# Performance work log

Hardware: AMD Instinct MI355X
Metric: run time of the kernel (lower is better)

## Reference

```python
import jax, jax.numpy as jnp
import numpy as np

B, S, NB, ORDER, D = 256, 50, 8, 2, 128
N_ITEMS, N_RELS = 100000, 200
STDV = 1.0 / float(np.sqrt(D))  # reset_parameters: uniform(-1/sqrt(hidden), 1/sqrt(hidden))


def setup_inputs() -> dict:
    key = jax.random.key(0)
    ks = jax.random.split(key, 24)
    u = lambda k, shape: jax.random.uniform(k, shape, jnp.float32, -STDV, STDV)
    return {
        'h_iids': jax.random.randint(ks[0], (B, S), 1, N_ITEMS),
        'a_iids': jax.random.randint(ks[1], (B,), 0, N_ITEMS),
        'adj_entity': jax.random.randint(ks[2], (N_ITEMS, NB), 0, N_ITEMS),
        'adj_relation': jax.random.randint(ks[3], (N_ITEMS, NB), 0, N_RELS),
        'item_emb': u(ks[4], (N_ITEMS, D)),
        'rel_emb': u(ks[5], (N_RELS, D)),
        'Wa': u(ks[6], (D, 1)), 'ba': u(ks[7], (1,)),          # linear_attention
        'Wt': u(ks[8], (D, D)), 'bt': u(ks[9], (D,)),          # linear_attention_transform
        'Wih': u(ks[10], (D, 3 * D)), 'Whh': u(ks[11], (D, 3 * D)),  # GRU (1 layer)
        'bih': u(ks[12], (3 * D,)), 'bhh': u(ks[13], (3 * D,)),
        'W1': u(ks[14], (D, D)), 'b1': u(ks[15], (D,)),        # linear_one
        'W2': u(ks[16], (D, D)), 'b2': u(ks[17], (D,)),        # linear_two
        'W3': u(ks[18], (D, 1)),                               # linear_three (no bias)
        'Wtr': u(ks[19], (2 * D, D)), 'btr': u(ks[20], (D,)),  # linear_transform
    }


def _forward(h_iids, adj_entity, adj_relation, item_emb, rel_emb,
             Wa, ba, Wt, bt, Wih, Whh, bih, bhh,
             W1, b1, W2, b2, W3, Wtr, btr):
    # ---- get_neighbors: multi-hop KG neighbor expansion ----
    entities = [h_iids]           # level 0: [B, S]
    relations = []
    for i in range(ORDER):
        e = entities[i]
        entities.append(adj_entity[e].reshape(B, -1))    # [B, S*NB^(i+1)]
        relations.append(adj_relation[e].reshape(B, -1))
    ent_embs = [item_emb[e] for e in entities]           # gathers
    rel_embs = [rel_emb[r] for r in relations]
    # ---- high_order_aggregate: attention-weighted neighbor aggregation ----
    neib = ent_embs[ORDER]                                # [B, S*NB^ORDER, D]
    for i in range(ORDER):
        self_e = ent_embs[ORDER - i - 1]                  # [B, M, D]
        rel = rel_embs[ORDER - i - 1].reshape(B, -1, NB, D)
        nb4 = neib.reshape(rel.shape)                     # [B, M, NB, D]
        att = (self_e[:, :, None, :] * rel * nb4) @ Wa + ba   # [B, M, NB, 1]
        alpha = jax.nn.softmax(att, axis=2)
        agg = jnp.sum(nb4 * alpha, axis=2)                # [B, M, D]
        neib = (self_e + agg) @ Wt + bt                   # aggregate='sum' branch
    item_embs = neib                                      # [B, S, D] (sigmoid in src is dead code)
    # ---- GRU, 1 layer, batch_first ----
    def step(h, x):
        gi = x @ Wih + bih
        gh = h @ Whh + bhh
        ir, iz, inn = jnp.split(gi, 3, axis=-1)
        hr, hz, hn = jnp.split(gh, 3, axis=-1)
        r = jax.nn.sigmoid(ir + hr)
        z = jax.nn.sigmoid(iz + hz)
        n = jnp.tanh(inn + r * hn)
        h2 = (1.0 - z) * n + z * h
        return h2, h2
    h0 = jnp.zeros((B, D), jnp.float32)
    _, outs = jax.lax.scan(step, h0, jnp.swapaxes(item_embs, 0, 1))
    output = jnp.swapaxes(outs, 0, 1)                     # [B, S, D]
    # ---- attention pooling over sequence ----
    last_idx = jnp.clip(jnp.sum(h_iids != 0, axis=1) - 1, 0, S - 1)
    local_ht = output[jnp.arange(B), last_idx]            # [B, D]
    q1 = (local_ht @ W1 + b1)[:, None, :]
    q2 = output @ W2 + b2
    al = jax.nn.sigmoid(q1 + q2) @ W3                     # [B, S, 1]
    global_ht = jnp.sum(al * output, axis=1)
    ght = jnp.concatenate([local_ht, global_ht], axis=1) @ Wtr + btr
    logits = jax.nn.relu(ght @ item_emb.T)                # [B, n_items]
    return logits


def reference(h_iids, a_iids, adj_entity, adj_relation, item_emb, rel_emb,
              Wa, ba, Wt, bt, Wih, Whh, bih, bhh,
              W1, b1, W2, b2, W3, Wtr, btr):
    # a_iids is accepted by forward() but unused (matches the torch source).
    return _forward(h_iids, adj_entity, adj_relation, item_emb, rel_emb,
                    Wa, ba, Wt, bt, Wih, Whh, bih, bhh,
                    W1, b1, W2, b2, W3, Wtr, btr)
```

## Files before the change

### kernel.cpp

```cpp
#include <hip/hip_runtime.h>
#include <hip/hip_bf16.h>
#include <math.h>

#define NB_B 256
#define NB_S 50
#define NB_NB 8
#define NB_D 128
#define NB_NITEMS 100000

#define C_RZ (-1.442695041f)
#define C_N (2.885390082f)

typedef __attribute__((ext_vector_type(8))) short short8;
typedef __attribute__((ext_vector_type(4))) float f32x4;
typedef unsigned int uint;
typedef unsigned short ushort;

__device__ __forceinline__ ushort f2bf(float f) {
  union { float f; uint u; } v;
  v.f = f;
  return (ushort)((v.u + 0x7fffu + ((v.u >> 16) & 1u)) >> 16);
}
__device__ __forceinline__ uint packbf(float a, float b) {
  return (uint)f2bf(a) | ((uint)f2bf(b) << 16);
}
__device__ __forceinline__ float bflo(uint u) {
  union { uint u; float f; } v; v.u = u << 16; return v.f;
}
__device__ __forceinline__ float bfhi(uint u) {
  union { uint u; float f; } v; v.u = u & 0xffff0000u; return v.f;
}
__device__ __forceinline__ float bf2f(ushort u) {
  union { uint u; float f; } v; v.u = (uint)u << 16; return v.f;
}
__device__ __forceinline__ void unpack8(uint4 u, float* f) {
  f[0] = bflo(u.x); f[1] = bfhi(u.x);
  f[2] = bflo(u.y); f[3] = bfhi(u.y);
  f[4] = bflo(u.z); f[5] = bfhi(u.z);
  f[6] = bflo(u.w); f[7] = bfhi(u.w);
}

__device__ __forceinline__ void castf_body(const float* __restrict__ src,
                                           uint* __restrict__ dst, int i, int n8) {
  if (i >= n8) return;
  float4 a = ((const float4*)src)[2 * i];
  float4 b = ((const float4*)src)[2 * i + 1];
  uint4 o;
  o.x = packbf(a.x, a.y);
  o.y = packbf(a.z, a.w);
  o.z = packbf(b.x, b.y);
  o.w = packbf(b.z, b.w);
  ((uint4*)dst)[i] = o;
}
template <int CO, bool SCALED>
__device__ __forceinline__ void castT_body(const float* __restrict__ W,
                                           ushort* __restrict__ WT, int idx) {
  if (idx >= 128 * CO) return;
  int n = idx >> 7, k = idx & 127;
  float v = W[(size_t)k * CO + n];
  if (SCALED) v *= (n < 256 ? C_RZ : C_N);
  WT[idx] = f2bf(v);
}
__global__ __launch_bounds__(256) void prep_kernel(
    const float* __restrict__ item_emb, const float* __restrict__ rel_emb,
    const float* __restrict__ Wt, const float* __restrict__ Wih,
    const float* __restrict__ Whh, const float* __restrict__ W2,
    const float* __restrict__ bih, const float* __restrict__ bhh,
    const int* __restrict__ h_iids, const int* __restrict__ adj_e,
    const int* __restrict__ adj_r, uint* __restrict__ EMB_BF,
    uint* __restrict__ REL_BF, ushort* __restrict__ WtT,
    ushort* __restrict__ WihT, ushort* __restrict__ WhhT,
    ushort* __restrict__ W2T, float* __restrict__ GIBIAS,
    int* __restrict__ E0, int* __restrict__ E2, int* __restrict__ RK,
    int* __restrict__ RK1) {
  int bx = blockIdx.x, tid = threadIdx.x;
  if (bx < 6250) {
    castf_body(item_emb, EMB_BF, bx * 256 + tid, 1600000);
  } else if (bx < 6263) {
    castf_body(rel_emb, REL_BF, (bx - 6250) * 256 + tid, 3200);
  } else if (bx < 6327) {
    castT_body<128, false>(Wt, WtT, (bx - 6263) * 256 + tid);
  } else if (bx < 6519) {
    castT_body<384, true>(Wih, WihT, (bx - 6327) * 256 + tid);
  } else if (bx < 6711) {
    castT_body<384, true>(Whh, WhhT, (bx - 6519) * 256 + tid);
  } else if (bx < 6775) {
    castT_body<128, false>(W2, W2T, (bx - 6711) * 256 + tid);
  } else if (bx < 6776) {
    if (tid < 256) GIBIAS[tid] = C_RZ * (bih[tid] + bhh[tid]);
  } else if (bx < 6777) {
    int idx = 256 + tid;
    if (idx < 384) GIBIAS[idx] = C_N * bih[idx];
  } else if (bx < 7177) {
    int p = (bx - 6777) * 256 + tid;
    if (p < NB_B * NB_S * NB_NB) {
      int b = p / (NB_S * NB_NB);
      int m = p % (NB_S * NB_NB);
      int h = h_iids[b * NB_S + (m >> 3)];
      int e = adj_e[h * NB_NB + (m & 7)];
      E0[p] = e;
      int4 ea = ((const int4*)(adj_e + (size_t)e * 8))[0];
      int4 eb = ((const int4*)(adj_e + (size_t)e * 8))[1];
      int4 ra = ((const int4*)(adj_r + (size_t)e * 8))[0];
      int4 rb = ((const int4*)(adj_r + (size_t)e * 8))[1];
      ((int4*)(E2 + (size_t)p * 8))[0] = ea;
      ((int4*)(E2 + (size_t)p * 8))[1] = eb;
      ((int4*)(RK + (size_t)p * 8))[0] = ra;
      ((int4*)(RK + (size_t)p * 8))[1] = rb;
    }
  } else {
    int p = (bx - 7177) * 256 + tid;
    if (p < NB_B * NB_S) {
      int e = h_iids[p];
      int4 ra = ((const int4*)(adj_r + (size_t)e * 8))[0];
      int4 rb = ((const int4*)(adj_r + (size_t)e * 8))[1];
      ((int4*)(RK1 + (size_t)p * 8))[0] = ra;
      ((int4*)(RK1 + (size_t)p * 8))[1] = rb;
    }
  }
}

__device__ __forceinline__ uint4 hop_pair4(
    int e_self, int q, int p, const int* __restrict__ E2d,
    const int* __restrict__ RKd, const uint* __restrict__ embB,
    const uint* __restrict__ relB, const uint* __restrict__ neibB,
    const float* __restrict__ Wa, float* __restrict__ alds) {
  uint4 us = ((const uint4*)(embB + (size_t)e_self * 64))[q];
  float s[8], wa[8], sw[8];
  unpack8(us, s);
  *(float4*)&wa[0] = ((const float4*)Wa)[q * 2];
  *(float4*)&wa[4] = ((const float4*)Wa)[q * 2 + 1];
#pragma unroll
  for (int d = 0; d < 8; d++) sw[d] = s[d] * wa[d];

  int4 ra = ((const int4*)(RKd + (size_t)p * 8))[0];
  int4 rb = ((const int4*)(RKd + (size_t)p * 8))[1];
  int rk[8] = {ra.x, ra.y, ra.z, ra.w, rb.x, rb.y, rb.z, rb.w};

  uint4 nbp[8];
  if (neibB == nullptr) {
    int4 ea = ((const int4*)(E2d + (size_t)p * 8))[0];
    int4 eb = ((const int4*)(E2d + (size_t)p * 8))[1];
    int e2[8] = {ea.x, ea.y, ea.z, ea.w, eb.x, eb.y, eb.z, eb.w};
#pragma unroll
    for (int k = 0; k < 8; k++)
      nbp[k] = ((const uint4*)(embB + (size_t)e2[k] * 64))[q];
  } else {
#pragma unroll
    for (int k = 0; k < 8; k++)
      nbp[k] = ((const uint4*)(neibB + ((size_t)p * 8 + k) * 64))[q];
  }

  float t[8];
#pragma unroll
  for (int k = 0; k < 8; k++) {
    uint4 ur = ((const uint4*)(relB + (size_t)rk[k] * 64))[q];
    float rr[8], nb[8];
    unpack8(ur, rr);
    unpack8(nbp[k], nb);
    float tt = 0.f;
#pragma unroll
    for (int d = 0; d < 8; d++) tt = fmaf(sw[d] * rr[d], nb[d], tt);
    t[k] = tt;
  }

  bool b0 = (q & 1), b1 = (q & 2), b2 = (q & 4);
  float a4[4];
#pragma unroll
  for (int i = 0; i < 4; i++) {
    float send = b0 ? t[i] : t[4 + i];
    float recv = __shfl_xor(send, 1);
    a4[i] = (b0 ? t[4 + i] : t[i]) + recv;
  }
  float a2[2];
#pragma unroll
  for (int i = 0; i < 2; i++) {
    float send = b1 ? a4[i] : a4[2 + i];
    float recv = __shfl_xor(send, 2);
    a2[i] = (b1 ? a4[2 + i] : a4[i]) + recv;
  }
  float send1 = b2 ? a2[0] : a2[1];
  float recv1 = __shfl_xor(send1, 4);
  float c = (b2 ? a2[1] : a2[0]) + recv1;
  c += __shfl_xor(c, 8);

  float e = __expf(c);
  float den = e;
  den += __shfl_xor(den, 1);
  den += __shfl_xor(den, 2);
  den += __shfl_xor(den, 4);
  float alpha = e * __builtin_amdgcn_rcpf(den);

  int kstar = (q & 1) * 4 + (q & 2) + ((q & 4) >> 2);
  if (q < 8) alds[kstar] = alpha;
  asm volatile("s_waitcnt lgkmcnt(0)" ::: "memory");
  float a8[8];
  *(float4*)&a8[0] = ((const float4*)alds)[0];
  *(float4*)&a8[4] = ((const float4*)alds)[1];

  float x[8];
#pragma unroll
  for (int d = 0; d < 8; d++) x[d] = s[d];
#pragma unroll
  for (int k = 0; k < 8; k++) {
    float nb[8];
    unpack8(nbp[k], nb);
#pragma unroll
    for (int d = 0; d < 8; d++) x[d] = fmaf(a8[k], nb[d], x[d]);
  }
  uint4 o;
  o.x = packbf(x[0], x[1]);
  o.y = packbf(x[2], x[3]);
  o.z = packbf(x[4], x[5]);
  o.w = packbf(x[6], x[7]);
  return o;
}

__global__ __launch_bounds__(256) void hoplin_kernel(
    const int* __restrict__ E0, const int* __restrict__ E2,
    const int* __restrict__ RK, const uint* __restrict__ embB,
    const uint* __restrict__ relB, const float* __restrict__ Wa,
    const ushort* __restrict__ WtT, const float* __restrict__ bt,
    ushort* __restrict__ NEIB) {
  __shared__ ushort X0s[16 * 128];
  __shared__ float als[16][8];
  const int bx = blockIdx.x;
  const int wv = threadIdx.x >> 6, ln = threadIdx.x & 63;
  const int g = ln >> 4, q = ln & 15;
  const int lp = wv * 4 + g;
  const int p = bx * 16 + lp;

  int e_self = E0[p];
  uint4 o = hop_pair4(e_self, q, p, E2, RK, embB, relB, nullptr, Wa, als[lp]);
  {
    int byte = (lp * 256 + q * 16) ^ ((lp & 7) << 4);
    *(uint4*)((char*)X0s + byte) = o;
  }
  __syncthreads();

  const int lr = ln & 15, lg = ln >> 4;
  short8 afr[4];
#pragma unroll
  for (int kf = 0; kf < 4; kf++) {
    int byte = (lr * 256 + lg * 16 + kf * 64) ^ ((lr & 7) << 4);
    afr[kf] = *(const short8*)((const char*)X0s + byte);
  }
  f32x4 acc[2] = {};
#pragma unroll
  for (int nf = 0; nf < 2; nf++) {
    int n = (wv * 2 + nf) * 16 + lr;
    const ushort* bb = WtT + (size_t)n * 128 + lg * 8;
#pragma unroll
    for (int kf = 0; kf < 4; kf++) {
      short8 bv = *(const short8*)(bb + kf * 32);
      acc[nf] = __builtin_amdgcn_mfma_f32_16x16x32_bf16(afr[kf], bv, acc[nf],
                                                        0, 0, 0);
    }
  }
#pragma unroll
  for (int nf = 0; nf < 2; nf++) {
    int n = (wv * 2 + nf) * 16 + lr;
    float bv = bt[n];
#pragma unroll
    for (int r = 0; r < 4; r++) {
      int mg = bx * 16 + lg * 4 + r;
      NEIB[(size_t)mg * 128 + n] = f2bf(acc[nf][r] + bv);
    }
  }
}

__global__ __launch_bounds__(256) void hopgi_kernel(
    const int* __restrict__ h_iids, const int* __restrict__ RK1,
    const uint* __restrict__ embB, const uint* __restrict__ relB,
    const uint* __restrict__ neibB, const float* __restrict__ Wa,
    const ushort* __restrict__ WtT, const float* __restrict__ bt,
    const ushort* __restrict__ WihT, const float* __restrict__ GIBIAS,
    float* __restrict__ GI) {
  __shared__ ushort X1s[16 * 128];
  __shared__ ushort SEQs[16 * 128];
  __shared__ float als[16][8];
  const int wv = threadIdx.x >> 6, ln = threadIdx.x & 63;
  const int g = ln >> 4, q = ln & 15;
  const int lp = wv * 4 + g;
  const int p = blockIdx.x * 16 + lp;

  int e_self = h_iids[p];
  uint4 o = hop_pair4(e_self, q, p, nullptr, RK1, embB, relB, neibB, Wa, als[lp]);
  {
    int byte = (lp * 256 + q * 16) ^ ((lp & 7) << 4);
    *(uint4*)((char*)X1s + byte) = o;
  }
  __syncthreads();

  const int lr = ln & 15, lg = ln >> 4;
  {
    short8 afr[4];
#pragma unroll
    for (int kf = 0; kf < 4; kf++) {
      int byte = (lr * 256 + lg * 16 + kf * 64) ^ ((lr & 7) << 4);
      afr[kf] = *(const short8*)((const char*)X1s + byte);
    }
    f32x4 acc[2] = {};
#pragma unroll
    for (int nf = 0; nf < 2; nf++) {
      int n = (wv * 2 + nf) * 16 + lr;
      const ushort* bb = WtT + (size_t)n * 128 + lg * 8;
#pragma unroll
      for (int kf = 0; kf < 4; kf++) {
        short8 b = *(const short8*)(bb + kf * 32);
        acc[nf] = __builtin_amdgcn_mfma_f32_16x16x32_bf16(afr[kf], b, acc[nf],
                                                          0, 0, 0);
      }
    }
#pragma unroll
    for (int nf = 0; nf < 2; nf++) {
      int n = (wv * 2 + nf) * 16 + lr;
      float bv = bt[n];
#pragma unroll
      for (int r = 0; r < 4; r++) {
        int m = lg * 4 + r;
        int byte = (m * 256 + n * 2) ^ ((m & 7) << 4);
        *(ushort*)((char*)SEQs + byte) = f2bf(acc[nf][r] + bv);
      }
    }
  }
  __syncthreads();

  {
    short8 sfr[4];
#pragma unroll
    for (int kf = 0; kf < 4; kf++) {
      int byte = (lr * 256 + lg * 16 + kf * 64) ^ ((lr & 7) << 4);
      sfr[kf] = *(const short8*)((const char*)SEQs + byte);
    }
#pragma unroll
    for (int i = 0; i < 6; i++) {
      int n = (wv * 6 + i) * 16 + lr;
      const ushort* bb = WihT + (size_t)n * 128 + lg * 8;
      f32x4 a2 = {};
#pragma unroll
      for (int kf = 0; kf < 4; kf++) {
        short8 b = *(const short8*)(bb + kf * 32);
        a2 = __builtin_amdgcn_mfma_f32_16x16x32_bf16(sfr[kf], b, a2, 0, 0, 0);
      }
      float bv = GIBIAS[n];
#pragma unroll
      for (int r = 0; r < 4; r++) {
        int m = lg * 4 + r;
        GI[(size_t)(blockIdx.x * 16 + m) * 384 + n] = a2[r] + bv;
      }
    }
  }
}

__global__ __launch_bounds__(512) void gru_mfma_kernel(
    const float* __restrict__ GI, const ushort* __restrict__ WhhT_bf,
    const float* __restrict__ bhh, ushort* __restrict__ OUTB) {
  const int b0 = blockIdx.x * 16;
  const int tid = threadIdx.x;
  const int w = tid >> 6, ln = tid & 63;
  const int lr = ln & 15, lg = ln >> 4;
  const int j = w * 16 + lr;

  __shared__ ushort hA[16 * 128];
  __shared__ ushort hB[16 * 128];

  short8 bfr[3][4];
#pragma unroll
  for (int g = 0; g < 3; g++) {
    const ushort* bb = WhhT_bf + (size_t)(g * 128 + j) * 128 + lg * 8;
#pragma unroll
    for (int kf = 0; kf < 4; kf++) bfr[g][kf] = *(const short8*)(bb + kf * 32);
  }
  const float bhn = C_N * bhh[256 + j];

  float h_reg[4] = {0.f, 0.f, 0.f, 0.f};

  {
    uint* hz = (uint*)hA;
#pragma unroll
    for (int i = tid; i < 1024; i += 512) hz[i] = 0;
  }
  __syncthreads();

  float girA[4][3], girB[4][3], girC[4][3], girD[4][3];
#pragma unroll
  for (int r = 0; r < 4; r++) {
    const float* g0 = GI + ((size_t)(b0 + lg * 4 + r) * NB_S + 0) * 384 + j;
    girA[r][0] = g0[0]; girA[r][1] = g0[128]; girA[r][2] = g0[256];
    const float* g1 = GI + ((size_t)(b0 + lg * 4 + r) * NB_S + 1) * 384 + j;
    girB[r][0] = g1[0]; girB[r][1] = g1[128]; girB[r][2] = g1[256];
    const float* g2 = GI + ((size_t)(b0 + lg * 4 + r) * NB_S + 2) * 384 + j;
    girC[r][0] = g2[0]; girC[r][1] = g2[128]; girC[r][2] = g2[256];
  }

  auto STEP = [&](int t, ushort* hRead, ushort* hWrite, float (&cur)[4][3],
                  float (&pre3)[4][3]) {
    if (t + 3 < NB_S) {
#pragma unroll
      for (int r = 0; r < 4; r++) {
        const float* g = GI + ((size_t)(b0 + lg * 4 + r) * NB_S + (t + 3)) * 384 + j;
        pre3[r][0] = g[0]; pre3[r][1] = g[128]; pre3[r][2] = g[256];
      }
    }
    __builtin_amdgcn_sched_barrier(0);
    short8 afr[4];
#pragma unroll
    for (int kf = 0; kf < 4; kf++) {
      int byte = (lr * 256 + kf * 64 + lg * 16) ^ ((lr & 7) << 4);
      afr[kf] = *(const short8*)((const char*)hRead + byte);
    }
    f32x4 acc[3] = {};
#pragma unroll
    for (int g = 0; g < 3; g++)
#pragma unroll
      for (int kf = 0; kf < 4; kf++)
        acc[g] = __builtin_amdgcn_mfma_f32_16x16x32_bf16(afr[kf], bfr[g][kf],
                                                         acc[g], 0, 0, 0);
#pragma unroll
    for (int r = 0; r < 4; r++) {
      int b = lg * 4 + r;
      float rg = __builtin_amdgcn_rcpf(
          1.f + __builtin_amdgcn_exp2f(cur[r][0] + acc[0][r]));
      float ze = __builtin_amdgcn_exp2f(cur[r][1] + acc[1][r]);
      float xp = cur[r][2] + rg * (bhn + acc[2][r]);
      float e2 = __builtin_amdgcn_exp2f(xp);
      float n = 1.f - 2.f * __builtin_amdgcn_rcpf(e2 + 1.f);
      float h2 = n + (h_reg[r] - n) * __builtin_amdgcn_rcpf(1.f + ze);
      h_reg[r] = h2;
      ushort hb = f2bf(h2);
      OUTB[((size_t)(b0 + b) * NB_S + t) * 128 + j] = hb;
      int byte = (b * 256 + j * 2) ^ ((b & 7) << 4);
      *(ushort*)((char*)hWrite + byte) = hb;
    }
    asm volatile("s_waitcnt lgkmcnt(0)" ::: "memory");
    __builtin_amdgcn_s_barrier();
  };

  for (int g4 = 0; g4 < 12; g4++) {
    int t = g4 * 4;
    STEP(t + 0, hA, hB, girA, girD);
    STEP(t + 1, hB, hA, girB, girA);
    STEP(t + 2, hA, hB, girC, girB);
    STEP(t + 3, hB, hA, girD, girC);
  }
  STEP(48, hA, hB, girA, girD);
  STEP(49, hB, hA, girB, girA);
}

__global__ __launch_bounds__(256) void pool_kernel(
    const int* __restrict__ h_iids, const ushort* __restrict__ OUTB,
    const float* __restrict__ W1, const float* __restrict__ b1,
    const ushort* __restrict__ W2T, const float* __restrict__ b2,
    const float* __restrict__ W3, const float* __restrict__ Wtr,
    const float* __restrict__ btr, ushort* __restrict__ GHT_bf) {
  const int b = blockIdx.x, tid = threadIdx.x;
  __shared__ float lh[128];
  __shared__ float q1[128];
  __shared__ float al[64];
  __shared__ float cat[256];

  if (tid < 128) {
    int cnt = 0;
    for (int s = 0; s < NB_S; s++) cnt += (h_iids[b * NB_S + s] != 0);
    int li = min(max(cnt - 1, 0), NB_S - 1);
    lh[tid] = bf2f(OUTB[((size_t)b * NB_S + li) * 128 + tid]);
  }
  __syncthreads();
  if (tid < 128) {
    float acc = b1[tid];
    for (int d = 0; d < 128; d++) acc += lh[d] * W1[(size_t)d * 128 + tid];
    q1[tid] = acc;
  }
  __syncthreads();

  {
    const int wv = tid >> 6, ln = tid & 63, lr = ln & 15, lg = ln >> 4;
    const int s0 = wv * 16;
    short8 zz = {0, 0, 0, 0, 0, 0, 0, 0};
    short8 afr[4];
    int srow = s0 + lr;
#pragma unroll
    for (int kf = 0; kf < 4; kf++)
      afr[kf] = (srow < NB_S)
                    ? *(const short8*)(OUTB + ((size_t)b * NB_S + srow) * 128 +
                                       lg * 8 + kf * 32)
                    : zz;
    float part[4] = {0.f, 0.f, 0.f, 0.f};
#pragma unroll
    for (int nf = 0; nf < 8; nf++) {
      const ushort* bb = W2T + (size_t)(nf * 16 + lr) * 128 + lg * 8;
      f32x4 acc = {};
#pragma unroll
      for (int kf = 0; kf < 4; kf++) {
        short8 bv = *(const short8*)(bb + kf * 32);
        acc = __builtin_amdgcn_mfma_f32_16x16x32_bf16(afr[kf], bv, acc, 0, 0, 0);
      }
      int c = nf * 16 + lr;
      float qc = q1[c] + b2[c];
      float w3 = W3[c];
#pragma unroll
      for (int r = 0; r < 4; r++)
        part[r] += w3 / (1.f + __expf(-(qc + acc[r])));
    }
#pragma unroll
    for (int r = 0; r < 4; r++) {
#pragma unroll
      for (int off = 1; off < 16; off <<= 1) part[r] += __shfl_xor(part[r], off);
      int s = s0 + lg * 4 + r;
      if (lr == 0 && s < NB_S) al[s] = part[r];
    }
  }
  __syncthreads();

  if (tid < 128) {
    float g = 0.f;
    for (int s = 0; s < NB_S; s++)
      g += al[s] * bf2f(OUTB[((size_t)b * NB_S + s) * 128 + tid]);
    cat[tid] = lh[tid];
    cat[128 + tid] = g;
  }
  __syncthreads();
  if (tid < 128) {
    float acc = btr[tid];
    for (int dd = 0; dd < 256; dd++) acc += cat[dd] * Wtr[(size_t)dd * 128 + tid];
    GHT_bf[b * 128 + tid] = f2bf(acc);
  }
}

__global__ __launch_bounds__(256) void logits_mfma_kernel(
    const ushort* __restrict__ GHT_bf, const ushort* __restrict__ embB,
    float* __restrict__ out) {
  const int wv = threadIdx.x >> 6, ln = threadIdx.x & 63;
  const int lr = ln & 15, lg = ln >> 4;
  const int n0 = blockIdx.x * 128;
  const int m0 = wv * 64;

  short8 afr[4][4];
#pragma unroll
  for (int mf = 0; mf < 4; mf++) {
    const ushort* ab = GHT_bf + (size_t)(m0 + mf * 16 + lr) * 128 + lg * 8;
#pragma unroll
    for (int kf = 0; kf < 4; kf++) afr[mf][kf] = *(const short8*)(ab + kf * 32);
  }

  f32x4 acc[4][8] = {};
#pragma unroll
  for (int nf = 0; nf < 8; nf++) {
    int n = n0 + nf * 16 + lr;
    int nc = min(n, NB_NITEMS - 1);
    const ushort* bb = embB + (size_t)nc * 128 + lg * 8;
    short8 b0_[4];
#pragma unroll
    for (int kf = 0; kf < 4; kf++) b0_[kf] = *(const short8*)(bb + kf * 32);
#pragma unroll
    for (int mf = 0; mf < 4; mf++)
#pragma unroll
      for (int kf = 0; kf < 4; kf++)
        acc[mf][nf] = __builtin_amdgcn_mfma_f32_16x16x32_bf16(
            afr[mf][kf], b0_[kf], acc[mf][nf], 0, 0, 0);
  }

#pragma unroll
  for (int mf = 0; mf < 4; mf++)
#pragma unroll
    for (int r = 0; r < 4; r++) {
      int m = m0 + mf * 16 + lg * 4 + r;
#pragma unroll
      for (int nf = 0; nf < 8; nf++) {
        int n = n0 + nf * 16 + lr;
        if (n < NB_NITEMS)
          out[(size_t)m * NB_NITEMS + n] = fmaxf(acc[mf][nf][r], 0.f);
      }
    }
}

extern "C" void kernel_launch(void* const* d_in, const int* in_sizes, int n_in,
                              void* d_out, int out_size, void* d_ws, size_t ws_size,
                              hipStream_t stream) {
  const int* h_iids = (const int*)d_in[0];
  const int* adj_e = (const int*)d_in[2];
  const int* adj_r = (const int*)d_in[3];
  const float* item_emb = (const float*)d_in[4];
  const float* rel_emb = (const float*)d_in[5];
  const float* Wa = (const float*)d_in[6];
  const float* Wt = (const float*)d_in[8];
  const float* bt = (const float*)d_in[9];
  const float* Wih = (const float*)d_in[10];
  const float* Whh = (const float*)d_in[11];
  const float* bih = (const float*)d_in[12];
  const float* bhh = (const float*)d_in[13];
  const float* W1 = (const float*)d_in[14];
  const float* b1 = (const float*)d_in[15];
  const float* W2 = (const float*)d_in[16];
  const float* b2 = (const float*)d_in[17];
  const float* W3 = (const float*)d_in[18];
  const float* Wtr = (const float*)d_in[19];
  const float* btr = (const float*)d_in[20];
  float* out = (float*)d_out;

  char* w = (char*)d_ws;
  uint* EMB_BF = (uint*)w;                    w += 25600000;
  uint* REL_BF = (uint*)w;                    w += 51200;
  ushort* WtT_bf = (ushort*)w;                w += 32768;
  ushort* WihT_bf = (ushort*)w;               w += 98304;
  ushort* WhhT_bf = (ushort*)w;               w += 98304;
  ushort* W2T_bf = (ushort*)w;                w += 32768;
  float* GIBIAS = (float*)w;                  w += 2048;
  int* E0 = (int*)w;                          w += 409600;
  int* E2 = (int*)w;                          w += 3276800;
  int* RK = (int*)w;                          w += 3276800;
  int* RK1 = (int*)w;                         w += 409600;
  uint* NEIB_bf = (uint*)w;                   w += 26214400;
  float* GI = (float*)w;                      w += 19660800;
  ushort* OUTB = (ushort*)w;                  w += 3276800;
  ushort* GHT_bf = (ushort*)w;                w += 65536;

  prep_kernel<<<7227, 256, 0, stream>>>(item_emb, rel_emb, Wt, Wih, Whh, W2,
                                        bih, bhh, h_iids, adj_e, adj_r, EMB_BF,
                                        REL_BF, WtT_bf, WihT_bf, WhhT_bf,
                                        W2T_bf, GIBIAS, E0, E2, RK, RK1);

  hoplin_kernel<<<6400, 256, 0, stream>>>(E0, E2, RK, EMB_BF, REL_BF, Wa,
                                          WtT_bf, bt, (ushort*)NEIB_bf);
  hopgi_kernel<<<800, 256, 0, stream>>>(h_iids, RK1, EMB_BF, REL_BF, NEIB_bf,
                                        Wa, WtT_bf, bt, WihT_bf, GIBIAS, GI);

  gru_mfma_kernel<<<16, 512, 0, stream>>>(GI, WhhT_bf, bhh, OUTB);
  pool_kernel<<<256, 256, 0, stream>>>(h_iids, OUTB, W1, b1, W2T_bf, b2, W3,
                                       Wtr, btr, GHT_bf);

  logits_mfma_kernel<<<782, 256, 0, stream>>>(GHT_bf, (const ushort*)EMB_BF, out);
}
```

Before: 192.6 us.

## Process two 16-row batch tiles per GRU block to interleave independent MFMA chains

```diff
diff --git a/kernel.cpp b/kernel.cpp
--- a/kernel.cpp
+++ b/kernel.cpp
@@ -356,14 +356,14 @@
 __global__ __launch_bounds__(512) void gru_mfma_kernel(
     const float* __restrict__ GI, const ushort* __restrict__ WhhT_bf,
     const float* __restrict__ bhh, ushort* __restrict__ OUTB) {
-  const int b0 = blockIdx.x * 16;
+  const int b0 = blockIdx.x * 32;
   const int tid = threadIdx.x;
   const int w = tid >> 6, ln = tid & 63;
   const int lr = ln & 15, lg = ln >> 4;
   const int j = w * 16 + lr;
 
-  __shared__ ushort hA[16 * 128];
-  __shared__ ushort hB[16 * 128];
+  __shared__ ushort h0[2 * 2048];
+  __shared__ ushort h1[2 * 2048];
 
   short8 bfr[3][4];
 #pragma unroll
@@ -374,78 +374,102 @@
   }
   const float bhn = C_N * bhh[256 + j];
 
-  float h_reg[4] = {0.f, 0.f, 0.f, 0.f};
+  float hrA[4] = {0.f, 0.f, 0.f, 0.f};
+  float hrB[4] = {0.f, 0.f, 0.f, 0.f};
 
   {
-    uint* hz = (uint*)hA;
-#pragma unroll
-    for (int i = tid; i < 1024; i += 512) hz[i] = 0;
-  }
-  __syncthreads();
-
-  float girA[4][3], girB[4][3], girC[4][3], girD[4][3];
+    uint* hz = (uint*)h0;
+#pragma unroll
+    for (int i = tid; i < 2048; i += 512) hz[i] = 0;
+  }
+  __syncthreads();
+
+  float gA0[4][3], gA1[4][3], gA2[4][3];
+  float gB0[4][3], gB1[4][3], gB2[4][3];
 #pragma unroll
   for (int r = 0; r < 4; r++) {
-    const float* g0 = GI + ((size_t)(b0 + lg * 4 + r) * NB_S + 0) * 384 + j;
-    girA[r][0] = g0[0]; girA[r][1] = g0[128]; girA[r][2] = g0[256];
-    const float* g1 = GI + ((size_t)(b0 + lg * 4 + r) * NB_S + 1) * 384 + j;
-    girB[r][0] = g1[0]; girB[r][1] = g1[128]; girB[r][2] = g1[256];
-    const float* g2 = GI + ((size_t)(b0 + lg * 4 + r) * NB_S + 2) * 384 + j;
-    girC[r][0] = g2[0]; girC[r][1] = g2[128]; girC[r][2] = g2[256];
-  }
-
-  auto STEP = [&](int t, ushort* hRead, ushort* hWrite, float (&cur)[4][3],
-                  float (&pre3)[4][3]) {
-    if (t + 3 < NB_S) {
+    const float* a0 = GI + ((size_t)(b0 + lg * 4 + r) * NB_S + 0) * 384 + j;
+    gA0[r][0] = a0[0]; gA0[r][1] = a0[128]; gA0[r][2] = a0[256];
+    const float* a1 = GI + ((size_t)(b0 + lg * 4 + r) * NB_S + 1) * 384 + j;
+    gA1[r][0] = a1[0]; gA1[r][1] = a1[128]; gA1[r][2] = a1[256];
+    const float* c0 = GI + ((size_t)(b0 + 16 + lg * 4 + r) * NB_S + 0) * 384 + j;
+    gB0[r][0] = c0[0]; gB0[r][1] = c0[128]; gB0[r][2] = c0[256];
+    const float* c1 = GI + ((size_t)(b0 + 16 + lg * 4 + r) * NB_S + 1) * 384 + j;
+    gB1[r][0] = c1[0]; gB1[r][1] = c1[128]; gB1[r][2] = c1[256];
+  }
+
+  auto STEP2 = [&](int t, ushort* hR, ushort* hW, float (&curA)[4][3],
+                   float (&preA)[4][3], float (&curB)[4][3],
+                   float (&preB)[4][3]) {
+    if (t + 2 < NB_S) {
 #pragma unroll
       for (int r = 0; r < 4; r++) {
-        const float* g = GI + ((size_t)(b0 + lg * 4 + r) * NB_S + (t + 3)) * 384 + j;
-        pre3[r][0] = g[0]; pre3[r][1] = g[128]; pre3[r][2] = g[256];
+        const float* a = GI + ((size_t)(b0 + lg * 4 + r) * NB_S + (t + 2)) * 384 + j;
+        preA[r][0] = a[0]; preA[r][1] = a[128]; preA[r][2] = a[256];
+        const float* c =
+            GI + ((size_t)(b0 + 16 + lg * 4 + r) * NB_S + (t + 2)) * 384 + j;
+        preB[r][0] = c[0]; preB[r][1] = c[128]; preB[r][2] = c[256];
       }
     }
     __builtin_amdgcn_sched_barrier(0);
-    short8 afr[4];
+    short8 afrA[4], afrB[4];
 #pragma unroll
     for (int kf = 0; kf < 4; kf++) {
       int byte = (lr * 256 + kf * 64 + lg * 16) ^ ((lr & 7) << 4);
-      afr[kf] = *(const short8*)((const char*)hRead + byte);
-    }
-    f32x4 acc[3] = {};
+      afrA[kf] = *(const short8*)((const char*)hR + byte);
+      afrB[kf] = *(const short8*)((const char*)hR + 4096 + byte);
+    }
+    f32x4 accA[3] = {}, accB[3] = {};
 #pragma unroll
     for (int g = 0; g < 3; g++)
 #pragma unroll
-      for (int kf = 0; kf < 4; kf++)
-        acc[g] = __builtin_amdgcn_mfma_f32_16x16x32_bf16(afr[kf], bfr[g][kf],
-                                                         acc[g], 0, 0, 0);
+      for (int kf = 0; kf < 4; kf++) {
+        accA[g] = __builtin_amdgcn_mfma_f32_16x16x32_bf16(afrA[kf], bfr[g][kf],
+                                                          accA[g], 0, 0, 0);
+        accB[g] = __builtin_amdgcn_mfma_f32_16x16x32_bf16(afrB[kf], bfr[g][kf],
+                                                          accB[g], 0, 0, 0);
+      }
 #pragma unroll
     for (int r = 0; r < 4; r++) {
       int b = lg * 4 + r;
-      float rg = __builtin_amdgcn_rcpf(
-          1.f + __builtin_amdgcn_exp2f(cur[r][0] + acc[0][r]));
-      float ze = __builtin_amdgcn_exp2f(cur[r][1] + acc[1][r]);
-      float xp = cur[r][2] + rg * (bhn + acc[2][r]);
-      float e2 = __builtin_amdgcn_exp2f(xp);
-      float n = 1.f - 2.f * __builtin_amdgcn_rcpf(e2 + 1.f);
-      float h2 = n + (h_reg[r] - n) * __builtin_amdgcn_rcpf(1.f + ze);
-      h_reg[r] = h2;
-      ushort hb = f2bf(h2);
-      OUTB[((size_t)(b0 + b) * NB_S + t) * 128 + j] = hb;
+      float rgA = __builtin_amdgcn_rcpf(
+          1.f + __builtin_amdgcn_exp2f(curA[r][0] + accA[0][r]));
+      float zeA = __builtin_amdgcn_exp2f(curA[r][1] + accA[1][r]);
+      float xpA = curA[r][2] + rgA * (bhn + accA[2][r]);
+      float e2A = __builtin_amdgcn_exp2f(xpA);
+      float nA = 1.f - 2.f * __builtin_amdgcn_rcpf(e2A + 1.f);
+      float h2A = nA + (hrA[r] - nA) * __builtin_amdgcn_rcpf(1.f + zeA);
+      hrA[r] = h2A;
+      ushort hbA = f2bf(h2A);
+      OUTB[((size_t)(b0 + b) * NB_S + t) * 128 + j] = hbA;
       int byte = (b * 256 + j * 2) ^ ((b & 7) << 4);
-      *(ushort*)((char*)hWrite + byte) = hb;
+      *(ushort*)((char*)hW + byte) = hbA;
+      float rgB = __builtin_amdgcn_rcpf(
+          1.f + __builtin_amdgcn_exp2f(curB[r][0] + accB[0][r]));
+      float zeB = __builtin_amdgcn_exp2f(curB[r][1] + accB[1][r]);
+      float xpB = curB[r][2] + rgB * (bhn + accB[2][r]);
+      float e2B = __builtin_amdgcn_exp2f(xpB);
+      float nB = 1.f - 2.f * __builtin_amdgcn_rcpf(e2B + 1.f);
+      float h2B = nB + (hrB[r] - nB) * __builtin_amdgcn_rcpf(1.f + zeB);
+      hrB[r] = h2B;
+      ushort hbB = f2bf(h2B);
+      OUTB[((size_t)(b0 + 16 + b) * NB_S + t) * 128 + j] = hbB;
+      *(ushort*)((char*)hW + 4096 + byte) = hbB;
     }
     asm volatile("s_waitcnt lgkmcnt(0)" ::: "memory");
     __builtin_amdgcn_s_barrier();
   };
 
-  for (int g4 = 0; g4 < 12; g4++) {
-    int t = g4 * 4;
-    STEP(t + 0, hA, hB, girA, girD);
-    STEP(t + 1, hB, hA, girB, girA);
-    STEP(t + 2, hA, hB, girC, girB);
-    STEP(t + 3, hB, hA, girD, girC);
-  }
-  STEP(48, hA, hB, girA, girD);
-  STEP(49, hB, hA, girB, girA);
+  for (int g3 = 0; g3 < 16; g3++) {
+    int t = g3 * 3;
+    ushort* p0 = (g3 & 1) ? h1 : h0;
+    ushort* p1 = (g3 & 1) ? h0 : h1;
+    STEP2(t + 0, p0, p1, gA0, gA2, gB0, gB2);
+    STEP2(t + 1, p1, p0, gA1, gA0, gB1, gB0);
+    STEP2(t + 2, p0, p1, gA2, gA1, gB2, gB1);
+  }
+  STEP2(48, h0, h1, gA0, gA2, gB0, gB2);
+  STEP2(49, h1, h0, gA1, gA0, gB1, gB0);
 }
 
 __global__ __launch_bounds__(256) void pool_kernel(
@@ -626,7 +650,7 @@
   hopgi_kernel<<<800, 256, 0, stream>>>(h_iids, RK1, EMB_BF, REL_BF, NEIB_bf,
                                         Wa, WtT_bf, bt, WihT_bf, GIBIAS, GI);
 
-  gru_mfma_kernel<<<16, 512, 0, stream>>>(GI, WhhT_bf, bhh, OUTB);
+  gru_mfma_kernel<<<8, 512, 0, stream>>>(GI, WhhT_bf, bhh, OUTB);
   pool_kernel<<<256, 256, 0, stream>>>(h_iids, OUTB, W1, b1, W2T_bf, b2, W3,
                                        Wtr, btr, GHT_bf);
 
```

New measurement: 223.9 us. 1.16x slower.
